# Optimization experiments

Measured on AMD Instinct MI355X. Metric: run time of the kernel, lower is better.

The kernel has to match this reference:

```python
import jax, jax.numpy as jnp
import numpy as np

BETA = 0.25  # VQ commitment cost


def setup_inputs() -> dict:
    key = jax.random.key(0)
    ks = jax.random.split(key, 6)
    B, C, H, W = 4096, 10, 32, 32
    Din, D, K = 3 * H * W, 256, 512
    img = jax.random.normal(ks[0], (B, 3, H, W), jnp.float32)
    label = jax.random.randint(ks[1], (B,), 0, C)
    enc_W = jax.random.normal(ks[2], (C, Din, D), jnp.float32) * (1.0 / np.sqrt(Din))
    enc_b = jnp.zeros((C, D), jnp.float32)
    codebook = jax.random.normal(ks[3], (K, D), jnp.float32)
    dec_W = jax.random.normal(ks[4], (D, Din), jnp.float32) * (1.0 / np.sqrt(D))
    dec_b = jnp.zeros((Din,), jnp.float32)
    return {"img": img, "label": label, "enc_W": enc_W, "enc_b": enc_b,
            "codebook": codebook, "dec_W": dec_W, "dec_b": dec_b}


def reference(img, label, enc_W, enc_b, codebook, dec_W, dec_b):
    B = img.shape[0]
    C = enc_W.shape[0]
    x = img.reshape(B, -1)                                   # [B, Din]
    onehot = jax.nn.one_hot(label, C, dtype=x.dtype)         # [B, C]
    # label-routed per-class encoders: encode with every expert, select by label
    z_all = jnp.einsum('bi,cid->bcd', x, enc_W) + enc_b[None]  # [B, C, D]
    z = jnp.einsum('bcd,bc->bd', z_all, onehot)              # [B, D]
    # --- VQ quantizer (shared) ---
    d2 = (jnp.sum(z * z, -1, keepdims=True)
          - 2.0 * (z @ codebook.T)
          + jnp.sum(codebook * codebook, -1)[None])          # [B, K]
    idx = jnp.argmin(d2, axis=-1)                            # [B]
    q = codebook[idx]                                        # [B, D]
    # per-sample VQ loss (mean over latent dim): codebook + beta*commitment
    cb_l = jnp.mean((jax.lax.stop_gradient(z) - q) ** 2, -1)
    cm_l = jnp.mean((z - jax.lax.stop_gradient(q)) ** 2, -1)
    l = cb_l + BETA * cm_l                                   # [B]
    q_st = z + jax.lax.stop_gradient(q - z)                  # straight-through
    # quantization loss = (sum over activated classes of per-subset mean) / n_activated
    counts = jax.ops.segment_sum(jnp.ones((B,), x.dtype), label, num_segments=C)
    sum_l = jax.ops.segment_sum(l, label, num_segments=C)
    present = counts > 0
    per_class = jnp.where(present, sum_l / jnp.maximum(counts, 1.0), 0.0)
    n_act = jnp.maximum(jnp.sum(present.astype(x.dtype)), 1.0)
    quant = jnp.sum(per_class) / n_act
    # shared decoder; scatter-back is identity here since every label has an expert
    dec = q_st @ dec_W + dec_b                               # [B, Din]
    img_out = dec.reshape(img.shape)
    loss = jnp.mean((img_out - img) ** 2) + quant
    return (loss, img_out)
```

## Files before the change

### kernel.cpp

```cpp
#include <hip/hip_runtime.h>
#include <hip/hip_bf16.h>
#include <stddef.h>
#include <stdint.h>

#define NB   4096
#define NC   10
#define DIN  3072
#define DD   256
#define KCB  512
#define KSPLIT 8
#define KC   (DIN / KSPLIT)
#define TM   64
#define TGRID 80
#define NIT  (KC / 32)

#define PW_C  786432
#define PW_NH 393216
#define PW_KS 49152
#define PW_IT 4096

typedef unsigned short u16;
typedef short s16x8 __attribute__((ext_vector_type(8)));
typedef float f32x4 __attribute__((ext_vector_type(4)));

__device__ inline void f2bf2(float f, u16& h, u16& l) {
    unsigned uf = __builtin_bit_cast(unsigned, f);
    unsigned uh = (uf + 0x7FFFu + ((uf >> 16) & 1u)) >> 16;
    h = (u16)uh;
    float fh = __builtin_bit_cast(float, uh << 16);
    float r = f - fh;
    unsigned ur = __builtin_bit_cast(unsigned, r);
    l = (u16)((ur + 0x7FFFu + ((ur >> 16) & 1u)) >> 16);
}

__device__ __forceinline__ void gl16(const u16* g, u16* l) {
    __builtin_amdgcn_global_load_lds(
        (const __attribute__((address_space(1))) unsigned int*)(uintptr_t)g,
        (__attribute__((address_space(3))) unsigned int*)(unsigned int)(uintptr_t)l,
        16, 0, 0);
}

__global__ __launch_bounds__(256) void k_wtp(
    const int* __restrict__ label, const float* __restrict__ cb,
    const float* __restrict__ encW, const float* __restrict__ dW,
    int* __restrict__ meta, int* __restrict__ order, float* __restrict__ cbn,
    u16* __restrict__ WtH, u16* __restrict__ WtL,
    u16* __restrict__ dWtH, u16* __restrict__ dWtL, float* __restrict__ cbt)
{
    const int t = threadIdx.x;
    const int bid = blockIdx.x;
    if (bid == 0) {
        __shared__ int cnt_s[NC], cur_s[NC], off_s[NC];
        if (t < NC) { cnt_s[t] = 0; cur_s[t] = 0; }
        __syncthreads();
        for (int b = t; b < NB; b += 256) atomicAdd(&cnt_s[label[b]], 1);
        __syncthreads();
        if (t == 0) {
            int o = 0;
            for (int c = 0; c < NC; ++c) {
                off_s[c] = o; meta[c] = cnt_s[c]; meta[32 + c] = o; o += cnt_s[c];
            }
            meta[32 + NC] = o;
            int ntl = 0;
            for (int c = 0; c < NC; ++c)
                for (int r0 = 0; r0 < cnt_s[c]; r0 += TM) {
                    meta[64 + 2 * ntl] = c; meta[65 + 2 * ntl] = r0; ++ntl;
                }
            meta[63] = ntl;
        }
        __syncthreads();
        for (int b = t; b < NB; b += 256) {
            int c = label[b];
            int p = atomicAdd(&cur_s[c], 1);
            order[off_s[c] + p] = b;
        }
        return;
    }
    if (bid <= 2) {
        int k = (bid - 1) * 256 + t;
        if (k < KCB) {
            const float* r = cb + (size_t)k * DD;
            float a = 0.f;
#pragma unroll 4
            for (int i = 0; i < 64; ++i) {
                float4 v = *(const float4*)(r + i * 4);
                a = fmaf(v.x, v.x, fmaf(v.y, v.y, fmaf(v.z, v.z, fmaf(v.w, v.w, a))));
            }
            cbn[k] = a;
        }
        return;
    }
    const int wb = bid - 3;
    const float* src; int lsrc, ldst, k0, n0;
    u16 *dH = nullptr, *dL = nullptr; float* fdst = nullptr;
    int encw_c = -1;
    if (wb < 1920) {
        int c = wb / 192, rem = wb % 192;
        int kt = rem >> 2, nt = rem & 3;
        k0 = kt * 64; n0 = nt * 64;
        src = encW + (size_t)c * DIN * DD;  lsrc = DD;
        encw_c = c; ldst = 0;
    } else if (wb < 2112) {
        int rem = wb - 1920;
        int kt = rem / 48, nt = rem % 48;
        k0 = kt * 64; n0 = nt * 64;
        src = dW; lsrc = DIN;
        dH = dWtH; dL = dWtL; ldst = DD;
    } else {
        int rem = wb - 2112;
        int kt = rem >> 2, nt = rem & 3;
        k0 = kt * 64; n0 = nt * 64;
        src = cb; lsrc = DD;
        fdst = cbt; ldst = KCB;
    }
    __shared__ float tile[64][65];
    const int trow = t >> 4, tc4 = t & 15;
#pragma unroll
    for (int j = 0; j < 4; ++j) {
        int kk = trow * 4 + j;
        float4 v = *(const float4*)&src[(size_t)(k0 + kk) * lsrc + n0 + tc4 * 4];
        tile[kk][tc4 * 4 + 0] = v.x; tile[kk][tc4 * 4 + 1] = v.y;
        tile[kk][tc4 * 4 + 2] = v.z; tile[kk][tc4 * 4 + 3] = v.w;
    }
    __syncthreads();
    const int n = n0 + (t >> 2), q = t & 3;
    if (fdst) {
#pragma unroll
        for (int j = 0; j < 4; ++j) {
            float4 o = {tile[q * 16 + 4 * j + 0][n - n0], tile[q * 16 + 4 * j + 1][n - n0],
                        tile[q * 16 + 4 * j + 2][n - n0], tile[q * 16 + 4 * j + 3][n - n0]};
            *(float4*)&fdst[(size_t)n * ldst + k0 + q * 16 + 4 * j] = o;
        }
        return;
    }
    s16x8 vh0, vh1, vl0, vl1;
#pragma unroll
    for (int i = 0; i < 8; ++i) {
        u16 h, l;
        f2bf2(tile[q * 16 + i][n - n0], h, l);
        vh0[i] = (short)h; vl0[i] = (short)l;
    }
#pragma unroll
    for (int i = 0; i < 8; ++i) {
        u16 h, l;
        f2bf2(tile[q * 16 + 8 + i][n - n0], h, l);
        vh1[i] = (short)h; vl1[i] = (short)l;
    }
    if (encw_c >= 0) {
        const int nh = n >> 7, cg = (n & 127) >> 4, fr2 = n & 15;
        const size_t nbase = (size_t)encw_c * PW_C + (size_t)nh * PW_NH
                           + (size_t)cg * 512 + (size_t)fr2 * 8;
        int ko = (k0 >> 3) + 2 * q;
        {
            int ks2 = ko / 48, r2 = ko % 48, it2 = r2 >> 2, fg2 = r2 & 3;
            size_t o = nbase + (size_t)ks2 * PW_KS + (size_t)it2 * PW_IT + (size_t)fg2 * 128;
            *(s16x8*)&WtH[o] = vh0; *(s16x8*)&WtL[o] = vl0;
        }
        {
            int ko1 = ko + 1;
            int ks2 = ko1 / 48, r2 = ko1 % 48, it2 = r2 >> 2, fg2 = r2 & 3;
            size_t o = nbase + (size_t)ks2 * PW_KS + (size_t)it2 * PW_IT + (size_t)fg2 * 128;
            *(s16x8*)&WtH[o] = vh1; *(s16x8*)&WtL[o] = vl1;
        }
        return;
    }
    u16* oH = dH + (size_t)n * ldst + k0 + q * 16;
    u16* oL = dL + (size_t)n * ldst + k0 + q * 16;
    *(s16x8*)oH = vh0; *(s16x8*)(oH + 8) = vh1;
    *(s16x8*)oL = vl0; *(s16x8*)(oL + 8) = vl1;
}

__global__ __launch_bounds__(256, 2) void k_enc(
    const float* __restrict__ x, const u16* __restrict__ WpH, const u16* __restrict__ WpL,
    const int* __restrict__ order, const int* __restrict__ meta, float* __restrict__ zpart)
{
    const int bid = blockIdx.x;
    const int ks  = bid & 7;
    const int tid = bid >> 3;
    if (tid >= meta[63]) return;
    const int c    = meta[64 + 2 * tid];
    const int row0 = meta[65 + 2 * tid];
    const int cnt  = meta[c];
    const int off  = meta[32 + c];
    const int kbase = ks * KC;

    __shared__ __align__(16) u16 AsH[2048], AsL[2048];
    __shared__ __align__(16) u16 BsH[2][8192], BsL[2][8192];

    const int t = threadIdx.x;
    const int lane = t & 63;
    const int w    = t >> 6;
    const int fr = lane & 15, fg = lane >> 4;

    const int ar = ((t >> 6) << 4) | (t & 15);
    const int aq = (t >> 4) & 3;
    int lr = row0 + ar; if (lr > cnt - 1) lr = cnt - 1;
    const float* xp = x + (size_t)order[off + lr] * DIN + kbase + aq * 8;
    const int aoffs = t * 8;

    const u16* gchunk = ((w & 2) ? WpL : WpH)
                      + (size_t)c * PW_C + (size_t)(w & 1) * PW_NH
                      + (size_t)ks * PW_KS + lane * 8;
    u16* lchunk = ((w & 2) ? &BsL[0][0] : &BsH[0][0]) + (w & 1) * 4096;

    f32x4 acc[4][4];
#pragma unroll
    for (int i = 0; i < 4; ++i)
#pragma unroll
        for (int j = 0; j < 4; ++j) acc[i][j] = (f32x4){0.f, 0.f, 0.f, 0.f};

    auto cvt_store = [&](float4 a0, float4 a1) {
        float av[8] = {a0.x, a0.y, a0.z, a0.w, a1.x, a1.y, a1.z, a1.w};
        s16x8 vh, vl;
#pragma unroll
        for (int i = 0; i < 8; ++i) {
            u16 h, l; f2bf2(av[i], h, l);
            vh[i] = (short)h; vl[i] = (short)l;
        }
        *(s16x8*)&AsH[aoffs] = vh;
        *(s16x8*)&AsL[aoffs] = vl;
    };

    float4 pa0 = *(const float4*)xp;
    float4 pa1 = *(const float4*)(xp + 4);
#pragma unroll
    for (int i = 0; i < 8; ++i) gl16(gchunk + i * 512, lchunk + i * 512);
    cvt_store(pa0, pa1);

    const int arb = fg * 128 + fr * 8;
    const int brb = (w >> 1) * 4096 + (w & 1) * 2048 + arb;

    for (int it = 0; it < NIT; ++it) {
        const int pb = it & 1;
        __syncthreads();
        if (it + 1 < NIT) {
            const u16* g = gchunk + (size_t)(it + 1) * PW_IT;
            u16* l = lchunk + (pb ^ 1) * 8192;
#pragma unroll
            for (int i = 0; i < 8; ++i) gl16(g + i * 512, l + i * 512);
            pa0 = *(const float4*)(xp + (it + 1) * 32);
            pa1 = *(const float4*)(xp + (it + 1) * 32 + 4);
        }
        s16x8 aH[4], aL[4];
#pragma unroll
        for (int mt = 0; mt < 4; ++mt) {
            aH[mt] = *(const s16x8*)&AsH[mt * 512 + arb];
            aL[mt] = *(const s16x8*)&AsL[mt * 512 + arb];
        }
#pragma unroll
        for (int ct = 0; ct < 4; ++ct) {
            const int bo = pb * 8192 + ct * 512 + brb;
            s16x8 bH = *(const s16x8*)&(&BsH[0][0])[bo];
            s16x8 bL = *(const s16x8*)&(&BsL[0][0])[bo];
#pragma unroll
            for (int mt = 0; mt < 4; ++mt) {
                acc[mt][ct] = __builtin_amdgcn_mfma_f32_16x16x32_bf16(aH[mt], bH, acc[mt][ct], 0, 0, 0);
                acc[mt][ct] = __builtin_amdgcn_mfma_f32_16x16x32_bf16(aL[mt], bH, acc[mt][ct], 0, 0, 0);
                acc[mt][ct] = __builtin_amdgcn_mfma_f32_16x16x32_bf16(aH[mt], bL, acc[mt][ct], 0, 0, 0);
            }
        }
        __syncthreads();
        if (it + 1 < NIT) cvt_store(pa0, pa1);
    }

    float* zp = zpart + (size_t)ks * NB * DD;
#pragma unroll
    for (int mt = 0; mt < 4; ++mt) {
#pragma unroll
        for (int r = 0; r < 4; ++r) {
            int lrow = row0 + mt * 16 + fg * 4 + r;
            if (lrow < cnt) {
                int gb = order[off + lrow];
                float* dst = zp + (size_t)gb * DD + w * 64 + fr;
#pragma unroll
                for (int ct = 0; ct < 4; ++ct)
                    dst[ct * 16] = acc[mt][ct][r];
            }
        }
    }
}

__global__ __launch_bounds__(256, 3) void k_dec(
    const float* __restrict__ cb, const u16* __restrict__ dWtH, const u16* __restrict__ dWtL,
    const float* __restrict__ db, float* __restrict__ dcb)
{
    const int col0 = blockIdx.x * 256;
    const int m0   = blockIdx.y * 64;

    __shared__ u16 AsH[64 * 40], AsL[64 * 40], BsH[256 * 40], BsL[256 * 40];

    const int t = threadIdx.x;
    const int lane = t & 63;
    const int wid  = t >> 6;
    const int wr = wid >> 1, wc = wid & 1;

    const int ar = t >> 2, aq = t & 3;
    const float* ap = cb + (size_t)(m0 + ar) * DD + aq * 8;
    const int bc = t >> 1, bh = t & 1;
    const u16* wH0 = dWtH + (size_t)(col0 + bc) * DD + bh * 16;
    const u16* wH1 = wH0 + (size_t)128 * DD;
    const u16* wL0 = dWtL + (size_t)(col0 + bc) * DD + bh * 16;
    const u16* wL1 = wL0 + (size_t)128 * DD;

    f32x4 acc[2][8];
#pragma unroll
    for (int i = 0; i < 2; ++i)
#pragma unroll
        for (int j = 0; j < 8; ++j) acc[i][j] = (f32x4){0.f, 0.f, 0.f, 0.f};

    const int fr = lane & 15, fg = lane >> 4;
    const int aoff = fg * 8;
    const int awr = ar * 40 + aq * 8;
    const int bw0 = bc * 40 + bh * 16;
    const int bw1 = (bc + 128) * 40 + bh * 16;

    float4 pa0 = *(const float4*)(ap);
    float4 pa1 = *(const float4*)(ap + 4);
    s16x8 ph0 = *(const s16x8*)(wH0);
    s16x8 ph1 = *(const s16x8*)(wH0 + 8);
    s16x8 ph2 = *(const s16x8*)(wH1);
    s16x8 ph3 = *(const s16x8*)(wH1 + 8);
    s16x8 pl0 = *(const s16x8*)(wL0);
    s16x8 pl1 = *(const s16x8*)(wL0 + 8);
    s16x8 pl2 = *(const s16x8*)(wL1);
    s16x8 pl3 = *(const s16x8*)(wL1 + 8);

    for (int it = 0; it < DD / 32; ++it) {
        {
            float av[8] = {pa0.x, pa0.y, pa0.z, pa0.w, pa1.x, pa1.y, pa1.z, pa1.w};
            s16x8 vh, vl;
#pragma unroll
            for (int i = 0; i < 8; ++i) {
                u16 h, l; f2bf2(av[i], h, l);
                vh[i] = (short)h; vl[i] = (short)l;
            }
            *(s16x8*)&AsH[awr] = vh;
            *(s16x8*)&AsL[awr] = vl;
            *(s16x8*)&BsH[bw0]     = ph0;
            *(s16x8*)&BsH[bw0 + 8] = ph1;
            *(s16x8*)&BsH[bw1]     = ph2;
            *(s16x8*)&BsH[bw1 + 8] = ph3;
            *(s16x8*)&BsL[bw0]     = pl0;
            *(s16x8*)&BsL[bw0 + 8] = pl1;
            *(s16x8*)&BsL[bw1]     = pl2;
            *(s16x8*)&BsL[bw1 + 8] = pl3;
        }
        __syncthreads();
        if (it + 1 < DD / 32) {
            const int k0 = (it + 1) * 32;
            pa0 = *(const float4*)(ap + k0);
            pa1 = *(const float4*)(ap + k0 + 4);
            ph0 = *(const s16x8*)(wH0 + k0);
            ph1 = *(const s16x8*)(wH0 + k0 + 8);
            ph2 = *(const s16x8*)(wH1 + k0);
            ph3 = *(const s16x8*)(wH1 + k0 + 8);
            pl0 = *(const s16x8*)(wL0 + k0);
            pl1 = *(const s16x8*)(wL0 + k0 + 8);
            pl2 = *(const s16x8*)(wL1 + k0);
            pl3 = *(const s16x8*)(wL1 + k0 + 8);
        }
        s16x8 aH0 = *(const s16x8*)&AsH[(wr * 32 + fr) * 40 + aoff];
        s16x8 aH1 = *(const s16x8*)&AsH[(wr * 32 + 16 + fr) * 40 + aoff];
        s16x8 aL0 = *(const s16x8*)&AsL[(wr * 32 + fr) * 40 + aoff];
        s16x8 aL1 = *(const s16x8*)&AsL[(wr * 32 + 16 + fr) * 40 + aoff];
#pragma unroll
        for (int nt = 0; nt < 8; ++nt) {
            const int bcol = wc * 128 + nt * 16 + fr;
            s16x8 bH = *(const s16x8*)&BsH[bcol * 40 + aoff];
            s16x8 bL = *(const s16x8*)&BsL[bcol * 40 + aoff];
            acc[0][nt] = __builtin_amdgcn_mfma_f32_16x16x32_bf16(aH0, bH, acc[0][nt], 0, 0, 0);
            acc[0][nt] = __builtin_amdgcn_mfma_f32_16x16x32_bf16(aL0, bH, acc[0][nt], 0, 0, 0);
            acc[0][nt] = __builtin_amdgcn_mfma_f32_16x16x32_bf16(aH0, bL, acc[0][nt], 0, 0, 0);
            acc[1][nt] = __builtin_amdgcn_mfma_f32_16x16x32_bf16(aH1, bH, acc[1][nt], 0, 0, 0);
            acc[1][nt] = __builtin_amdgcn_mfma_f32_16x16x32_bf16(aL1, bH, acc[1][nt], 0, 0, 0);
            acc[1][nt] = __builtin_amdgcn_mfma_f32_16x16x32_bf16(aH1, bL, acc[1][nt], 0, 0, 0);
        }
        __syncthreads();
    }

#pragma unroll
    for (int mt = 0; mt < 2; ++mt) {
#pragma unroll
        for (int r = 0; r < 4; ++r) {
            int grow = m0 + wr * 32 + mt * 16 + fg * 4 + r;
            float* dst = dcb + (size_t)grow * DIN + col0 + wc * 128 + fr;
#pragma unroll
            for (int nt = 0; nt < 8; ++nt)
                dst[nt * 16] = acc[mt][nt][r] + db[col0 + wc * 128 + nt * 16 + fr];
        }
    }
}

__global__ __launch_bounds__(256) void k_zred(
    const float* __restrict__ zpart, const float* __restrict__ encB,
    const int* __restrict__ label, float* __restrict__ z, float* __restrict__ zn)
{
    int id = blockIdx.x * 256 + threadIdx.x;
    int b = id >> 6, c4 = id & 63;
    int lab = label[b];
    float4 s = *(const float4*)&encB[lab * DD + c4 * 4];
    const float* p = zpart + (size_t)b * DD + c4 * 4;
#pragma unroll
    for (int ks = 0; ks < KSPLIT; ++ks) {
        float4 v = *(const float4*)(p + (size_t)ks * NB * DD);
        s.x += v.x; s.y += v.y; s.z += v.z; s.w += v.w;
    }
    *(float4*)&z[(size_t)b * DD + c4 * 4] = s;
    float sq = fmaf(s.x, s.x, fmaf(s.y, s.y, fmaf(s.z, s.z, s.w * s.w)));
#pragma unroll
    for (int o = 32; o > 0; o >>= 1) sq += __shfl_down(sq, o, 64);
    if ((threadIdx.x & 63) == 0) zn[b] = sq;
}

__global__ __launch_bounds__(256) void k_vq(
    const float* __restrict__ z, const float* __restrict__ cbt, const float* __restrict__ cbn,
    float* __restrict__ vmin, int* __restrict__ vidx)
{
    const int sg = blockIdx.x >> 2;
    const int q  = blockIdx.x & 3;
    const int b0 = sg * 32;
    const int code0 = q * 128;

    __shared__ float As[32][36];
    __shared__ float Bs[32][132];

    const int t = threadIdx.x;
    const int tx = t & 31, ty = t >> 5;

    const int ar = t >> 3, akq = t & 7;
    const float* zp = z + (size_t)(b0 + ar) * DD + akq * 4;
    const int bkk = t >> 3, bcq = t & 7;
    const float* cp = cbt + (size_t)bkk * KCB + code0 + bcq * 16;

    float acc[4][4];
#pragma unroll
    for (int i = 0; i < 4; ++i)
#pragma unroll
        for (int j = 0; j < 4; ++j) acc[i][j] = 0.f;

    float4 pa  = *(const float4*)zp;
    float4 pb0 = *(const float4*)(cp);
    float4 pb1 = *(const float4*)(cp + 4);
    float4 pb2 = *(const float4*)(cp + 8);
    float4 pb3 = *(const float4*)(cp + 12);

    for (int it = 0; it < DD / 32; ++it) {
        As[akq * 4 + 0][ar] = pa.x;
        As[akq * 4 + 1][ar] = pa.y;
        As[akq * 4 + 2][ar] = pa.z;
        As[akq * 4 + 3][ar] = pa.w;
        *(float4*)&Bs[bkk][bcq * 16]      = pb0;
        *(float4*)&Bs[bkk][bcq * 16 + 4]  = pb1;
        *(float4*)&Bs[bkk][bcq * 16 + 8]  = pb2;
        *(float4*)&Bs[bkk][bcq * 16 + 12] = pb3;
        __syncthreads();
        if (it + 1 < DD / 32) {
            const float* zpn = zp + (it + 1) * 32;
            const float* cpn = cp + (size_t)(it + 1) * 32 * KCB;
            pa  = *(const float4*)zpn;
            pb0 = *(const float4*)(cpn);
            pb1 = *(const float4*)(cpn + 4);
            pb2 = *(const float4*)(cpn + 8);
            pb3 = *(const float4*)(cpn + 12);
        }
#pragma unroll
        for (int kk = 0; kk < 32; ++kk) {
            float4 a4 = *(const float4*)&As[kk][ty * 4];
            float4 b4 = *(const float4*)&Bs[kk][tx * 4];
            float am[4] = {a4.x, a4.y, a4.z, a4.w};
            float bn[4] = {b4.x, b4.y, b4.z, b4.w};
#pragma unroll
            for (int i = 0; i < 4; ++i)
#pragma unroll
                for (int j = 0; j < 4; ++j)
                    acc[i][j] = fmaf(am[i], bn[j], acc[i][j]);
        }
        __syncthreads();
    }

    float4 cn4 = *(const float4*)&cbn[code0 + tx * 4];
    float cnv[4] = {cn4.x, cn4.y, cn4.z, cn4.w};
#pragma unroll
    for (int i = 0; i < 4; ++i) {
        float m = cnv[0] - 2.f * acc[i][0];
        int bi = code0 + tx * 4;
#pragma unroll
        for (int j = 1; j < 4; ++j) {
            float sc = cnv[j] - 2.f * acc[i][j];
            if (sc < m) { m = sc; bi = code0 + tx * 4 + j; }
        }
#pragma unroll
        for (int mask = 1; mask <= 16; mask <<= 1) {
            float om = __shfl_xor(m, mask, 64);
            int   oi = __shfl_xor(bi, mask, 64);
            bool lowerSelf = (tx & mask) == 0;
            float lm = lowerSelf ? m : om;
            int   li = lowerSelf ? bi : oi;
            float hm = lowerSelf ? om : m;
            int   hi2 = lowerSelf ? oi : bi;
            if (hm < lm) { m = hm; bi = hi2; } else { m = lm; bi = li; }
        }
        if (tx == 0) {
            vmin[(size_t)(b0 + ty * 4 + i) * 4 + q] = m;
            vidx[(size_t)(b0 + ty * 4 + i) * 4 + q] = bi;
        }
    }
}

__global__ __launch_bounds__(256) void k_vqm(
    const float* __restrict__ vmin, const int* __restrict__ vidx, const float* __restrict__ zn,
    int* __restrict__ idxo, float* __restrict__ lo)
{
    int b = blockIdx.x * 256 + threadIdx.x;
    float m = vmin[b * 4]; int bi = vidx[b * 4];
#pragma unroll
    for (int q = 1; q < 4; ++q) {
        float v = vmin[b * 4 + q];
        if (v < m) { m = v; bi = vidx[b * 4 + q]; }
    }
    idxo[b] = bi;
    lo[b] = (zn[b] + m) * (1.25f / 256.f);
}

__global__ __launch_bounds__(256) void k_gather(
    const float* __restrict__ dcb, const int* __restrict__ idxo, const float* __restrict__ img,
    float* __restrict__ out1, float* __restrict__ ssep)
{
    const int b = blockIdx.x;
    const int k = idxo[b];
    const float* src = dcb + (size_t)k * DIN;
    const float* im  = img + (size_t)b * DIN;
    float* o = out1 + (size_t)b * DIN;
    const float4* s4 = (const float4*)src;
    const float4* i4 = (const float4*)im;

    float accv = 0.f;
#pragma unroll
    for (int j = 0; j < 3; ++j) {
        int i = threadIdx.x + j * 256;
        float4 v = s4[i], w = i4[i];
        float dx = v.x - w.x, dy = v.y - w.y, dz = v.z - w.z, dw = v.w - w.w;
        accv = fmaf(dx, dx, fmaf(dy, dy, fmaf(dz, dz, fmaf(dw, dw, accv))));
    }
#pragma unroll
    for (int j = 0; j < 3; ++j) {
        int i = threadIdx.x + j * 256;
        if (i < DIN / 4 - 1) {
            float4 a = s4[i], b2 = s4[i + 1];
            float4 ov = {a.w, b2.x, b2.y, b2.z};
            *(float4*)(o + 3 + 4 * i) = ov;
        }
    }
    if (threadIdx.x == 0) {
        o[0] = src[0]; o[1] = src[1]; o[2] = src[2];
        o[DIN - 1] = src[DIN - 1];
    }

    __shared__ float red[256];
    red[threadIdx.x] = accv;
    __syncthreads();
#pragma unroll
    for (int st = 128; st > 0; st >>= 1) {
        if (threadIdx.x < st) red[threadIdx.x] += red[threadIdx.x + st];
        __syncthreads();
    }
    if (threadIdx.x == 0) ssep[b] = red[0];
}

__global__ __launch_bounds__(256) void k_final(
    const float* __restrict__ ssep, const float* __restrict__ lo, const int* __restrict__ label,
    const int* __restrict__ meta, float* __restrict__ out)
{
    const int t = threadIdx.x;
    __shared__ float red[256];
    __shared__ float csum[NC];

    float se = 0.f;
    for (int b = t; b < NB; b += 256) se += ssep[b];

    float la[NC];
#pragma unroll
    for (int c = 0; c < NC; ++c) la[c] = 0.f;
    for (int b = t; b < NB; b += 256) {
        int c2 = label[b]; float v = lo[b];
#pragma unroll
        for (int cc = 0; cc < NC; ++cc) la[cc] += (cc == c2) ? v : 0.f;
    }

    red[t] = se; __syncthreads();
    for (int st = 128; st > 0; st >>= 1) { if (t < st) red[t] += red[t + st]; __syncthreads(); }
    float sse = red[0];
    __syncthreads();

    for (int cc = 0; cc < NC; ++cc) {
        red[t] = la[cc]; __syncthreads();
        for (int st = 128; st > 0; st >>= 1) { if (t < st) red[t] += red[t + st]; __syncthreads(); }
        if (t == 0) csum[cc] = red[0];
        __syncthreads();
    }

    if (t == 0) {
        float quant = 0.f, nact = 0.f;
        for (int cc = 0; cc < NC; ++cc) {
            int cnt = meta[cc];
            if (cnt > 0) { quant += csum[cc] / (float)cnt; nact += 1.f; }
        }
        if (nact < 1.f) nact = 1.f;
        quant /= nact;
        out[0] = sse / (float)(NB * DIN) + quant;
    }
}

extern "C" void kernel_launch(void* const* d_in, const int* in_sizes, int n_in,
                              void* d_out, int out_size, void* d_ws, size_t ws_size,
                              hipStream_t stream)
{
    const float* img   = (const float*)d_in[0];
    const int*   label = (const int*)d_in[1];
    const float* encW  = (const float*)d_in[2];
    const float* encB  = (const float*)d_in[3];
    const float* cb    = (const float*)d_in[4];
    const float* dW    = (const float*)d_in[5];
    const float* db    = (const float*)d_in[6];
    float* out = (float*)d_out;

    char* w = (char*)d_ws;
    float* zpart = (float*)(w);
    float* dcb   = (float*)(w);
    float* z     = (float*)(w + 33554432);
    u16*   WtH   = (u16*)  (w + 37748736);
    u16*   WtL   = (u16*)  (w + 53477376);
    u16*   dWtH  = (u16*)  (w + 69206016);
    u16*   dWtL  = (u16*)  (w + 70778880);
    float* vmin  = (float*)(w + 72351744);
    int*   vidx  = (int*)  (w + 72417280);
    float* zn    = (float*)(w + 72482816);
    float* lo    = (float*)(w + 72499200);
    float* ssep  = (float*)(w + 72515584);
    int*   idxo  = (int*)  (w + 72531968);
    int*   order = (int*)  (w + 72548352);
    int*   meta  = (int*)  (w + 72564736);
    float* cbn   = (float*)(w + 72568832);
    float* cbt   = (float*)(w + 72570880);

    hipLaunchKernelGGL(k_wtp,    dim3(2147),      dim3(256), 0, stream,
                       label, cb, encW, dW, meta, order, cbn, WtH, WtL, dWtH, dWtL, cbt);
    hipLaunchKernelGGL(k_enc,    dim3(TGRID * 8), dim3(256), 0, stream, img, WtH, WtL, order, meta, zpart);
    hipLaunchKernelGGL(k_zred,   dim3(1024),      dim3(256), 0, stream, zpart, encB, label, z, zn);
    hipLaunchKernelGGL(k_vq,     dim3(512),       dim3(256), 0, stream, z, cbt, cbn, vmin, vidx);
    hipLaunchKernelGGL(k_vqm,    dim3(16),        dim3(256), 0, stream, vmin, vidx, zn, idxo, lo);
    hipLaunchKernelGGL(k_dec,    dim3(12, 8),     dim3(256), 0, stream, cb, dWtH, dWtL, db, dcb);
    hipLaunchKernelGGL(k_gather, dim3(4096),      dim3(256), 0, stream, dcb, idxo, img, out + 1, ssep);
    hipLaunchKernelGGL(k_final,  dim3(1),         dim3(256), 0, stream, ssep, lo, label, meta, out);
}
```

Measured before the change: 147.9 us.

## Deepen encoder GEMM pipeline to prefetch two stages ahead with explicit waitcnts

```diff
diff --git a/kernel.cpp b/kernel.cpp
--- a/kernel.cpp
+++ b/kernel.cpp
@@ -170,6 +170,56 @@
     *(s16x8*)oL = vl0; *(s16x8*)(oL + 8) = vl1;
 }
 
+#define ENC_STEP(IT, PB, L0, L1, C0, C1)                                        \
+    {                                                                           \
+        if ((IT) + 1 < NIT) { asm volatile("s_waitcnt vmcnt(10)" ::: "memory"); } \
+        else                { asm volatile("s_waitcnt vmcnt(0)"  ::: "memory"); } \
+        asm volatile("s_waitcnt lgkmcnt(0)" ::: "memory");                      \
+        __builtin_amdgcn_s_barrier();                                           \
+        __builtin_amdgcn_sched_barrier(0);                                      \
+        s16x8 aH[4], aL[4], bH[4], bL[4];                                       \
+        _Pragma("unroll")                                                       \
+        for (int mt = 0; mt < 4; ++mt) {                                        \
+            aH[mt] = *(const s16x8*)&AsH[mt * 512 + arb];                       \
+            aL[mt] = *(const s16x8*)&AsL[mt * 512 + arb];                       \
+        }                                                                       \
+        _Pragma("unroll")                                                       \
+        for (int ct = 0; ct < 4; ++ct) {                                        \
+            bH[ct] = *(const s16x8*)&BsH[PB][ct * 512 + brb];                   \
+            bL[ct] = *(const s16x8*)&BsL[PB][ct * 512 + brb];                   \
+        }                                                                       \
+        asm volatile("s_waitcnt lgkmcnt(0)" ::: "memory");                      \
+        __builtin_amdgcn_sched_barrier(0);                                      \
+        __builtin_amdgcn_s_barrier();                                           \
+        __builtin_amdgcn_sched_barrier(0);                                      \
+        if ((IT) + 2 < NIT) {                                                   \
+            L0 = *(const float4*)(xp + ((IT) + 2) * 32);                        \
+            L1 = *(const float4*)(xp + ((IT) + 2) * 32 + 4);                    \
+            __builtin_amdgcn_sched_barrier(0);                                  \
+            const u16* g_ = gchunk + (size_t)((IT) + 2) * PW_IT;                \
+            u16* l_ = lchunk + (PB) * 8192;                                     \
+            _Pragma("unroll")                                                   \
+            for (int i = 0; i < 8; ++i) gl16(g_ + i * 512, l_ + i * 512);       \
+            __builtin_amdgcn_sched_barrier(0);                                  \
+        }                                                                       \
+        __builtin_amdgcn_s_setprio(1);                                          \
+        _Pragma("unroll")                                                       \
+        for (int ct = 0; ct < 4; ++ct) {                                        \
+            _Pragma("unroll")                                                   \
+            for (int mt = 0; mt < 4; ++mt) {                                    \
+                acc[mt][ct] = __builtin_amdgcn_mfma_f32_16x16x32_bf16(aH[mt], bH[ct], acc[mt][ct], 0, 0, 0); \
+                acc[mt][ct] = __builtin_amdgcn_mfma_f32_16x16x32_bf16(aL[mt], bH[ct], acc[mt][ct], 0, 0, 0); \
+                acc[mt][ct] = __builtin_amdgcn_mfma_f32_16x16x32_bf16(aH[mt], bL[ct], acc[mt][ct], 0, 0, 0); \
+            }                                                                   \
+        }                                                                       \
+        __builtin_amdgcn_s_setprio(0);                                          \
+        if ((IT) + 1 < NIT) {                                                   \
+            if ((IT) + 2 < NIT) { asm volatile("s_waitcnt vmcnt(18)" ::: "memory"); } \
+            else                { asm volatile("s_waitcnt vmcnt(8)"  ::: "memory"); } \
+            cvt_store(C0, C1);                                                  \
+        }                                                                       \
+    }
+
 __global__ __launch_bounds__(256, 2) void k_enc(
     const float* __restrict__ x, const u16* __restrict__ WpH, const u16* __restrict__ WpL,
     const int* __restrict__ order, const int* __restrict__ meta, float* __restrict__ zpart)
@@ -221,46 +271,30 @@
         *(s16x8*)&AsL[aoffs] = vl;
     };
 
-    float4 pa0 = *(const float4*)xp;
-    float4 pa1 = *(const float4*)(xp + 4);
-#pragma unroll
-    for (int i = 0; i < 8; ++i) gl16(gchunk + i * 512, lchunk + i * 512);
-    cvt_store(pa0, pa1);
-
     const int arb = fg * 128 + fr * 8;
     const int brb = (w >> 1) * 4096 + (w & 1) * 2048 + arb;
 
-    for (int it = 0; it < NIT; ++it) {
-        const int pb = it & 1;
-        __syncthreads();
-        if (it + 1 < NIT) {
-            const u16* g = gchunk + (size_t)(it + 1) * PW_IT;
-            u16* l = lchunk + (pb ^ 1) * 8192;
-#pragma unroll
-            for (int i = 0; i < 8; ++i) gl16(g + i * 512, l + i * 512);
-            pa0 = *(const float4*)(xp + (it + 1) * 32);
-            pa1 = *(const float4*)(xp + (it + 1) * 32 + 4);
-        }
-        s16x8 aH[4], aL[4];
-#pragma unroll
-        for (int mt = 0; mt < 4; ++mt) {
-            aH[mt] = *(const s16x8*)&AsH[mt * 512 + arb];
-            aL[mt] = *(const s16x8*)&AsL[mt * 512 + arb];
-        }
-#pragma unroll
-        for (int ct = 0; ct < 4; ++ct) {
-            const int bo = pb * 8192 + ct * 512 + brb;
-            s16x8 bH = *(const s16x8*)&(&BsH[0][0])[bo];
-            s16x8 bL = *(const s16x8*)&(&BsL[0][0])[bo];
-#pragma unroll
-            for (int mt = 0; mt < 4; ++mt) {
-                acc[mt][ct] = __builtin_amdgcn_mfma_f32_16x16x32_bf16(aH[mt], bH, acc[mt][ct], 0, 0, 0);
-                acc[mt][ct] = __builtin_amdgcn_mfma_f32_16x16x32_bf16(aL[mt], bH, acc[mt][ct], 0, 0, 0);
-                acc[mt][ct] = __builtin_amdgcn_mfma_f32_16x16x32_bf16(aH[mt], bL, acc[mt][ct], 0, 0, 0);
-            }
-        }
-        __syncthreads();
-        if (it + 1 < NIT) cvt_store(pa0, pa1);
+    float4 sa0, sa1, sb0, sb1;
+
+    sa0 = *(const float4*)xp;
+    sa1 = *(const float4*)(xp + 4);
+    __builtin_amdgcn_sched_barrier(0);
+#pragma unroll
+    for (int i = 0; i < 8; ++i) gl16(gchunk + i * 512, lchunk + i * 512);
+    __builtin_amdgcn_sched_barrier(0);
+    asm volatile("s_waitcnt vmcnt(8)" ::: "memory");
+    cvt_store(sa0, sa1);
+    __builtin_amdgcn_sched_barrier(0);
+    sb0 = *(const float4*)(xp + 32);
+    sb1 = *(const float4*)(xp + 36);
+    __builtin_amdgcn_sched_barrier(0);
+#pragma unroll
+    for (int i = 0; i < 8; ++i) gl16(gchunk + PW_IT + i * 512, lchunk + 8192 + i * 512);
+    __builtin_amdgcn_sched_barrier(0);
+
+    for (int itp = 0; itp < NIT; itp += 2) {
+        ENC_STEP(itp,     0, sa0, sa1, sb0, sb1);
+        ENC_STEP(itp + 1, 1, sb0, sb1, sa0, sa1);
     }
 
     float* zp = zpart + (size_t)ks * NB * DD;
```

After: 145.2 us. Within noise of the previous version (-1.8%).
